# Kernel tuning notes

Hardware: AMD Instinct MI355X
Metric: run time of the kernel (lower is better)

## Reference

```python
import jax, jax.numpy as jnp
import numpy as np

N_NODES = 100000
N_EDGES = 1600000
N_FEAT = 512
HIDDEN = 128
N_CLASSES = 64
K = 10
ALPHA = 0.1


def setup_inputs() -> dict:
    key = jax.random.key(0)
    k1, k2, k3, k4 = jax.random.split(key, 4)
    x = jax.random.normal(k1, (N_NODES, N_FEAT), dtype=jnp.float32)
    edge_index = jax.random.randint(k2, (2, N_EDGES), 0, N_NODES, dtype=jnp.int64)
    W1 = jax.random.normal(k3, (N_FEAT, HIDDEN), dtype=jnp.float32) * (1.0 / np.sqrt(N_FEAT))
    b1 = jnp.zeros((HIDDEN,), dtype=jnp.float32)
    W2 = jax.random.normal(k4, (HIDDEN, N_CLASSES), dtype=jnp.float32) * (1.0 / np.sqrt(HIDDEN))
    b2 = jnp.zeros((N_CLASSES,), dtype=jnp.float32)
    return {"x": x, "edge_index": edge_index, "W1": W1, "b1": b1, "W2": W2, "b2": b2}


def reference(x, edge_index, W1, b1, W2, b2):
    N = x.shape[0]
    # MLP (dropout disabled in eval): relu(x W1 + b1) W2 + b2
    h = jax.nn.relu(x @ W1 + b1) @ W2 + b2  # [N, C]

    # GCN normalization with self-loops (APPNP default)
    loop = jnp.arange(N, dtype=edge_index.dtype)
    src = jnp.concatenate([edge_index[0], loop])  # message sources
    dst = jnp.concatenate([edge_index[1], loop])  # message targets
    deg = jax.ops.segment_sum(jnp.ones_like(src, dtype=h.dtype), dst, num_segments=N)
    dinv = jnp.where(deg > 0, jax.lax.rsqrt(deg), 0.0)
    w = (dinv[src] * dinv[dst])[:, None]  # [E+N, 1] symmetric norm

    # K-step personalized-pagerank propagation with teleport mixing
    x0 = h
    for _ in range(K):
        agg = jax.ops.segment_sum(w * h[src], dst, num_segments=N)  # \hat{A} h
        h = (1.0 - ALPHA) * agg + ALPHA * x0

    return jax.nn.log_softmax(h, axis=1)
```

## Files before the change

kernel.cpp:

```cpp
#include <hip/hip_runtime.h>
#include <hip/hip_bf16.h>

typedef __attribute__((ext_vector_type(8))) short s8v;
typedef __attribute__((ext_vector_type(4))) float f4v;

#define NNODES 100000
#define NEDGES 1600000
#define NFEAT 512
#define NHID 128
#define NCLS 64
#define NBUK 196
#define CAP 9216

static __device__ __forceinline__ short f2bf(float f) {
  __hip_bfloat16 h = __float2bfloat16(f);
  return __builtin_bit_cast(short, h);
}
static __device__ __forceinline__ float bflo(unsigned int u) {
  return __builtin_bit_cast(float, u << 16);
}
static __device__ __forceinline__ float bfhi(unsigned int u) {
  return __builtin_bit_cast(float, u & 0xFFFF0000u);
}
static __device__ __forceinline__ unsigned int pk(float lo, float hi) {
  return (unsigned int)(unsigned short)f2bf(lo) |
         ((unsigned int)(unsigned short)f2bf(hi) << 16);
}
static __device__ __forceinline__ void glds16(const void* g, void* l) {
  __builtin_amdgcn_global_load_lds(
      (const __attribute__((address_space(1))) unsigned int*)g,
      (__attribute__((address_space(3))) unsigned int*)l, 16, 0, 0);
}

static __device__ __forceinline__ bool detect32(const int* __restrict__ ei, int* sm) {
  if (threadIdx.x == 0) *sm = 0;
  __syncthreads();
  int i = threadIdx.x & 255;
  int acc = ei[2 * i + 1] | ei[2 * (i + 256) + 1] |
            ei[2 * (i + 512) + 1] | ei[2 * (i + 768) + 1];
  if (acc != 0) atomicOr(sm, 1);
  __syncthreads();
  return *sm != 0;
}

__global__ __launch_bounds__(256) void bucket_k(const int* __restrict__ ei,
                                                int* __restrict__ gcur,
                                                uint2* __restrict__ pairbuf) {
  __shared__ int sm;
  __shared__ int lcnt[NBUK], gpos[NBUK], loff[NBUK];
  bool is32 = detect32(ei, &sm);
  int t = threadIdx.x;
  int e0 = blockIdx.x * 4096;
  if (t < NBUK) lcnt[t] = 0;
  __syncthreads();
  int s_[16], d_[16];
#pragma unroll
  for (int k = 0; k < 16; ++k) {
    int e = e0 + k * 256 + t;
    int s = -1, d = -1;
    if (e < NEDGES) {
      if (is32) { s = ei[e];     d = ei[NEDGES + e]; }
      else      { s = ei[2 * e]; d = ei[2 * NEDGES + 2 * e]; }
    }
    s_[k] = s; d_[k] = d;
    if (d >= 0) atomicAdd(&lcnt[d >> 9], 1);
  }
  __syncthreads();
  if (t < NBUK) { gpos[t] = atomicAdd(&gcur[t], lcnt[t]); loff[t] = 0; }
  __syncthreads();
#pragma unroll
  for (int k = 0; k < 16; ++k) {
    int d = d_[k];
    if (d >= 0) {
      int b = d >> 9;
      int pos = gpos[b] + atomicAdd(&loff[b], 1);
      if (pos < (b + 1) * CAP) {
        uint2 p; p.x = (unsigned)s_[k]; p.y = (unsigned)d;
        pairbuf[pos] = p;
      }
    }
  }
}

__global__ __launch_bounds__(1024) void csr_k(const uint2* __restrict__ pairbuf,
                                              const int* __restrict__ gcur,
                                              int* __restrict__ rs,
                                              float* __restrict__ dinv,
                                              int* __restrict__ csrc) {
  __shared__ int lcnt[512];
  __shared__ int lscan[512];
  __shared__ int ssz[256];
  int t = threadIdx.x, b = blockIdx.x;
  int nbase = b * 512;
  if (t < 256) ssz[t] = (t < NBUK) ? (gcur[t] - t * CAP) : 0;
  if (t < 512) lcnt[t] = 0;
  __syncthreads();
  for (int off = 1; off < 256; off <<= 1) {
    int v = 0;
    if (t < 256 && t >= off) v = ssz[t - off];
    __syncthreads();
    if (t < 256) ssz[t] += v;
    __syncthreads();
  }
  int nb = gcur[b] - b * CAP;
  int gbase = (b > 0) ? ssz[b - 1] : 0;
  const uint2* mybuf = pairbuf + (size_t)b * CAP;

  for (int i = t; i < nb; i += 1024)
    atomicAdd(&lcnt[mybuf[i].y & 511], 1);
  __syncthreads();

  int c0 = (t < 512) ? lcnt[t] : 0;
  if (t < 512) lscan[t] = c0;
  __syncthreads();
  for (int off = 1; off < 512; off <<= 1) {
    int v = 0;
    if (t < 512 && t >= off) v = lscan[t - off];
    __syncthreads();
    if (t < 512) lscan[t] += v;
    __syncthreads();
  }
  int node = nbase + t;
  int r0 = 0;
  if (t < 512) {
    r0 = gbase + lscan[t] - c0;
    if (node < NNODES) { rs[node] = r0; dinv[node] = rsqrtf((float)(c0 + 1)); }
  }
  if (b == NBUK - 1 && t == 0) rs[NNODES] = NEDGES;
  __syncthreads();
  if (t < 512) lcnt[t] = r0;
  __syncthreads();

  for (int i = t; i < nb; i += 1024) {
    uint2 p = mybuf[i];
    int pos = atomicAdd(&lcnt[p.y & 511], 1);
    csrc[pos] = (int)p.x;
  }
}

__global__ __launch_bounds__(256) void wt_k(const float* __restrict__ W1, short* __restrict__ W1t,
                                            const float* __restrict__ W2, short* __restrict__ W2t,
                                            int* __restrict__ gcur) {
  if (blockIdx.x == 0 && threadIdx.x < NBUK) gcur[threadIdx.x] = threadIdx.x * CAP;
  int i = blockIdx.x * 256 + threadIdx.x;
  if (i < NFEAT * NHID) {
    int k = i >> 7, c = i & 127;
    W1t[(size_t)c * NFEAT + k] = f2bf(W1[i]);
  } else {
    int j = i - NFEAT * NHID;
    if (j < NHID * NCLS) {
      int k = j >> 6, c = j & 63;
      W2t[(size_t)c * NHID + k] = f2bf(W2[j]);
    }
  }
}

__global__ __launch_bounds__(512, 4) void mlp3_k(const float* __restrict__ x,
                                                 const short* __restrict__ W1t,
                                                 const float* __restrict__ b1,
                                                 const short* __restrict__ W2t,
                                                 const float* __restrict__ b2,
                                                 const float* __restrict__ dinv,
                                                 unsigned short* __restrict__ x0,
                                                 unsigned short* __restrict__ g0) {
  __shared__ __align__(16) short As[2][8192];
  __shared__ __align__(16) short Bs[2][8192];
  int tid = threadIdx.x, lane = tid & 63, wave = tid >> 6;
  int r = lane & 15, q = lane >> 4;
  int G = tid >> 4, li = tid & 15;
  int row0 = blockIdx.x * 128;
  int wr = (wave >> 1) * 32, wc = (wave & 1) * 64;
  char* AsB = (char*)As;
  char* BsB = (char*)Bs;

  auto loadA = [&](float4* av, int kk) {
#pragma unroll
    for (int rd = 0; rd < 4; ++rd) {
      int row = rd * 32 + G;
      int grow = row0 + row; if (grow >= NNODES) grow = NNODES - 1;
      av[rd] = *reinterpret_cast<const float4*>(x + (size_t)grow * NFEAT + kk + li * 4);
    }
  };
  auto writeA = [&](const float4* av, int buf) {
#pragma unroll
    for (int rd = 0; rd < 4; ++rd) {
      int row = rd * 32 + G;
      uint2 u;
      u.x = pk(av[rd].x, av[rd].y);
      u.y = pk(av[rd].z, av[rd].w);
      *(uint2*)(AsB + buf * 16384 + row * 128 + (((li >> 1) ^ (row & 7)) << 4) + (li & 1) * 8) = u;
    }
  };
  auto stageB = [&](int buf, int kk) {
#pragma unroll
    for (int i2 = 0; i2 < 2; ++i2) {
      int i = wave * 2 + i2;
      int col = i * 8 + (lane >> 3);
      int srcg = (lane & 7) ^ (col & 7);
      glds16(W1t + (size_t)col * NFEAT + kk + srcg * 8, BsB + buf * 16384 + i * 1024);
    }
  };

  f4v acc[2][4];
#pragma unroll
  for (int a = 0; a < 2; ++a)
#pragma unroll
    for (int b = 0; b < 4; ++b) acc[a][b] = (f4v){0.f, 0.f, 0.f, 0.f};

  {
    float4 av[4];
    loadA(av, 0);
    stageB(0, 0);
    writeA(av, 0);
  }
  __syncthreads();

  int cur = 0;
  for (int c = 0; c < 8; ++c) {
    float4 av[4];
    if (c < 7) {
      loadA(av, (c + 1) * 64);
      stageB(cur ^ 1, (c + 1) * 64);
    }
#pragma unroll
    for (int kc = 0; kc < 2; ++kc) {
      s8v af[2], bfr[4];
#pragma unroll
      for (int rt = 0; rt < 2; ++rt) {
        int arow = wr + rt * 16 + r;
        af[rt] = *(const s8v*)(AsB + cur * 16384 + arow * 128 +
                               (((kc * 4 + q) ^ (arow & 7)) << 4));
      }
#pragma unroll
      for (int ct = 0; ct < 4; ++ct) {
        int bcol = wc + ct * 16 + r;
        bfr[ct] = *(const s8v*)(BsB + cur * 16384 + bcol * 128 +
                                (((kc * 4 + q) ^ (bcol & 7)) << 4));
      }
#pragma unroll
      for (int rt = 0; rt < 2; ++rt)
#pragma unroll
        for (int ct = 0; ct < 4; ++ct)
          acc[rt][ct] = __builtin_amdgcn_mfma_f32_16x16x32_bf16(af[rt], bfr[ct], acc[rt][ct], 0, 0, 0);
    }
    if (c < 7) writeA(av, cur ^ 1);
    __syncthreads();
    cur ^= 1;
  }

  {
    float bias1[4];
#pragma unroll
    for (int ct = 0; ct < 4; ++ct) bias1[ct] = b1[wc + ct * 16 + r];
#pragma unroll
    for (int rt = 0; rt < 2; ++rt)
#pragma unroll
      for (int ct = 0; ct < 4; ++ct) {
        int col = wc + ct * 16 + r;
#pragma unroll
        for (int j = 0; j < 4; ++j) {
          int row = wr + rt * 16 + q * 4 + j;
          float v = acc[rt][ct][j] + bias1[ct];
          v = v > 0.f ? v : 0.f;
          *(short*)(AsB + row * 256 + (((col >> 3) ^ (row & 15)) << 4) + (col & 7) * 2) = f2bf(v);
        }
      }
  }
  __syncthreads();

  int wc2 = (wave & 1) * 32;
  f4v acc2[2][2];
#pragma unroll
  for (int a = 0; a < 2; ++a)
#pragma unroll
    for (int b = 0; b < 2; ++b) acc2[a][b] = (f4v){0.f, 0.f, 0.f, 0.f};
#pragma unroll
  for (int kc = 0; kc < 4; ++kc) {
    s8v a2[2], b2f[2];
#pragma unroll
    for (int rt = 0; rt < 2; ++rt) {
      int row = wr + rt * 16 + r;
      a2[rt] = *(const s8v*)(AsB + row * 256 + (((kc * 4 + q) ^ (row & 15)) << 4));
    }
#pragma unroll
    for (int ct = 0; ct < 2; ++ct) {
      int col2 = wc2 + ct * 16 + r;
      b2f[ct] = *(const s8v*)(W2t + (size_t)col2 * NHID + kc * 32 + q * 8);
    }
#pragma unroll
    for (int rt = 0; rt < 2; ++rt)
#pragma unroll
      for (int ct = 0; ct < 2; ++ct)
        acc2[rt][ct] = __builtin_amdgcn_mfma_f32_16x16x32_bf16(a2[rt], b2f[ct], acc2[rt][ct], 0, 0, 0);
  }

  {
    float bias2[2];
#pragma unroll
    for (int ct = 0; ct < 2; ++ct) bias2[ct] = b2[wc2 + ct * 16 + r];
#pragma unroll
    for (int rt = 0; rt < 2; ++rt)
#pragma unroll
      for (int j = 0; j < 4; ++j) {
        int row = wr + rt * 16 + q * 4 + j;
        int grow = row0 + row;
        float dv = dinv[grow < NNODES ? grow : NNODES - 1];
#pragma unroll
        for (int ct = 0; ct < 2; ++ct) {
          float hh = acc2[rt][ct][j] + bias2[ct];
          int col = wc2 + ct * 16 + r;
          int byte = row * 128 + (((col >> 3) ^ (row & 7)) << 4) + (col & 7) * 2;
          *(short*)(BsB + byte) = f2bf(hh);
          *(short*)(BsB + 16384 + byte) = f2bf(dv * hh);
        }
      }
  }
  __syncthreads();
#pragma unroll
  for (int rd = 0; rd < 4; ++rd) {
    int row = rd * 32 + G;
    int grow = row0 + row;
    if (grow < NNODES) {
      int byte = row * 128 + (((li >> 1) ^ (row & 7)) << 4) + (li & 1) * 8;
      uint2 vx = *(const uint2*)(BsB + byte);
      uint2 vg = *(const uint2*)(BsB + 16384 + byte);
      *(uint2*)(x0 + (size_t)grow * NCLS + li * 4) = vx;
      *(uint2*)(g0 + (size_t)grow * NCLS + li * 4) = vg;
    }
  }
}

__global__ __launch_bounds__(256) void prop_k(const unsigned short* __restrict__ gin,
                                              const unsigned short* __restrict__ x0,
                                              const float* __restrict__ dinv,
                                              const int* __restrict__ rs,
                                              const int* __restrict__ csrc,
                                              unsigned short* __restrict__ gout,
                                              float* __restrict__ out,
                                              int last) {
  int tid = threadIdx.x;
  int lane = tid & 63;
  int r = lane & 7;
  int gbase = lane & 56;
  int node = blockIdx.x * 32 + (tid >> 6) * 8 + (lane >> 3);
  int b = rs[node];
  int deg = rs[node + 1] - b;

  uint4 sv = ((const uint4*)(gin + (size_t)node * NCLS))[r];
  uint4 xv = ((const uint4*)(x0 + (size_t)node * NCLS))[r];
  float dvn = dinv[node];

  float a0 = bflo(sv.x), a1 = bfhi(sv.x), a2 = bflo(sv.y), a3 = bfhi(sv.y);
  float a4 = bflo(sv.z), a5 = bfhi(sv.z), a6 = bflo(sv.w), a7 = bfhi(sv.w);

  int m = deg;
  m = max(m, __shfl_xor(m, 8));
  m = max(m, __shfl_xor(m, 16));
  m = max(m, __shfl_xor(m, 32));

  int idx = NNODES;
  if (r < deg) idx = csrc[b + r];
  for (int basek = 0; basek < m; basek += 8) {
    int nidx = NNODES;
    if (basek + 8 + r < deg) nidx = csrc[b + basek + 8 + r];
#pragma unroll
    for (int j = 0; j < 8; ++j) {
      int sj = __shfl(idx, gbase + j);
      uint4 v = ((const uint4*)(gin + (size_t)sj * NCLS))[r];
      a0 += bflo(v.x); a1 += bfhi(v.x); a2 += bflo(v.y); a3 += bfhi(v.y);
      a4 += bflo(v.z); a5 += bfhi(v.z); a6 += bflo(v.w); a7 += bfhi(v.w);
    }
    idx = nidx;
  }

  float h0 = 0.9f * (dvn * a0) + 0.1f * bflo(xv.x);
  float h1 = 0.9f * (dvn * a1) + 0.1f * bfhi(xv.x);
  float h2 = 0.9f * (dvn * a2) + 0.1f * bflo(xv.y);
  float h3 = 0.9f * (dvn * a3) + 0.1f * bfhi(xv.y);
  float h4 = 0.9f * (dvn * a4) + 0.1f * bflo(xv.z);
  float h5 = 0.9f * (dvn * a5) + 0.1f * bfhi(xv.z);
  float h6 = 0.9f * (dvn * a6) + 0.1f * bflo(xv.w);
  float h7 = 0.9f * (dvn * a7) + 0.1f * bfhi(xv.w);

  if (!last) {
    uint4 o;
    o.x = pk(dvn * h0, dvn * h1);
    o.y = pk(dvn * h2, dvn * h3);
    o.z = pk(dvn * h4, dvn * h5);
    o.w = pk(dvn * h6, dvn * h7);
    ((uint4*)(gout + (size_t)node * NCLS))[r] = o;
  } else {
    float mx = fmaxf(fmaxf(fmaxf(h0, h1), fmaxf(h2, h3)),
                     fmaxf(fmaxf(h4, h5), fmaxf(h6, h7)));
#pragma unroll
    for (int off = 1; off < 8; off <<= 1) mx = fmaxf(mx, __shfl_xor(mx, off));
    float s = __expf(h0 - mx) + __expf(h1 - mx) + __expf(h2 - mx) + __expf(h3 - mx) +
              __expf(h4 - mx) + __expf(h5 - mx) + __expf(h6 - mx) + __expf(h7 - mx);
#pragma unroll
    for (int off = 1; off < 8; off <<= 1) s += __shfl_xor(s, off);
    float ls = __logf(s);
    float* op = out + (size_t)node * NCLS + r * 8;
    float4 o0 = {h0 - mx - ls, h1 - mx - ls, h2 - mx - ls, h3 - mx - ls};
    float4 o1 = {h4 - mx - ls, h5 - mx - ls, h6 - mx - ls, h7 - mx - ls};
    *(float4*)(op) = o0;
    *(float4*)(op + 4) = o1;
  }
}

extern "C" void kernel_launch(void* const* d_in, const int* in_sizes, int n_in,
                              void* d_out, int out_size, void* d_ws, size_t ws_size,
                              hipStream_t stream) {
  const float* x  = (const float*)d_in[0];
  const int*   ei = (const int*)d_in[1];
  const float* W1 = (const float*)d_in[2];
  const float* b1 = (const float*)d_in[3];
  const float* W2 = (const float*)d_in[4];
  const float* b2 = (const float*)d_in[5];

  char* ws = (char*)d_ws;
  unsigned short* x0bf   = (unsigned short*)(ws);
  uint2*          pairbuf= (uint2*)(ws);
  unsigned short* gA     = (unsigned short*)(ws + 12800000);
  unsigned short* gB     = (unsigned short*)(ws + 25600256);
  int*            csrc   = (int*)(ws + 38400384);
  int*            rs     = (int*)(ws + 45200384);
  float*          dinv   = (float*)(ws + 46000512);
  short*          W1t    = (short*)(ws + 46800512);
  short*          W2t    = (short*)(ws + 46931584);
  int*            gcur   = (int*)(ws + 46950144);

  hipMemsetAsync((char*)gA + (size_t)NNODES * NCLS * 2, 0, 128, stream);
  hipMemsetAsync((char*)gB + (size_t)NNODES * NCLS * 2, 0, 128, stream);

  wt_k<<<(NFEAT * NHID + NHID * NCLS + 255) / 256, 256, 0, stream>>>(W1, W1t, W2, W2t, gcur);
  bucket_k<<<(NEDGES + 4095) / 4096, 256, 0, stream>>>(ei, gcur, pairbuf);
  csr_k<<<NBUK, 1024, 0, stream>>>(pairbuf, gcur, rs, dinv, csrc);

  mlp3_k<<<(NNODES + 127) / 128, 512, 0, stream>>>(x, W1t, b1, W2t, b2, dinv, x0bf, gB);

  for (int t = 1; t <= 10; ++t) {
    const unsigned short* gin = (t & 1) ? gB : gA;
    unsigned short* gout      = (t & 1) ? gA : gB;
    prop_k<<<NNODES / 32, 256, 0, stream>>>(gin, x0bf, dinv, rs, csrc, gout,
                                            (float*)d_out, t == 10);
  }
}
```

Before: 404.5 us.

## Split propagation features into 16-column blocks for cache-resident gathers

Reorganizes the bf16 propagation buffers into four column blocks of 16 features per node, and assigns each prop block one column block so that the gathered working set (about 3.2 MB per block) fits better in L2/MALL. Each node is now handled by two lanes with 16-byte loads, and the edge index reads are split across those two lanes. The log-softmax is moved into a separate kernel that reads the final bf16 state, and the padding memsets are folded into the weight transpose kernel. In exchange, each edge's index is now read four times (once per column block), and there is an extra launch plus a bf16 rounding of the final state before the softmax.

```diff
diff --git a/kernel.cpp b/kernel.cpp
--- a/kernel.cpp
+++ b/kernel.cpp
@@ -11,6 +11,7 @@
 #define NCLS 64
 #define NBUK 196
 #define CAP 9216
+#define CBS ((NNODES + 1) * 16)
 
 static __device__ __forceinline__ short f2bf(float f) {
   __hip_bfloat16 h = __float2bfloat16(f);
@@ -140,8 +141,16 @@
 
 __global__ __launch_bounds__(256) void wt_k(const float* __restrict__ W1, short* __restrict__ W1t,
                                             const float* __restrict__ W2, short* __restrict__ W2t,
-                                            int* __restrict__ gcur) {
+                                            int* __restrict__ gcur,
+                                            unsigned short* __restrict__ gA,
+                                            unsigned short* __restrict__ gB) {
   if (blockIdx.x == 0 && threadIdx.x < NBUK) gcur[threadIdx.x] = threadIdx.x * CAP;
+  if (blockIdx.x == 1 && threadIdx.x < 128) {
+    int t = threadIdx.x;
+    unsigned short* p = (t >> 6) ? gB : gA;
+    int c = (t >> 4) & 3, sh = t & 15;
+    p[(size_t)c * CBS + (size_t)NNODES * 16 + sh] = 0;
+  }
   int i = blockIdx.x * 256 + threadIdx.x;
   if (i < NFEAT * NHID) {
     int k = i >> 7, c = i & 127;
@@ -324,8 +333,9 @@
       int byte = row * 128 + (((li >> 1) ^ (row & 7)) << 4) + (li & 1) * 8;
       uint2 vx = *(const uint2*)(BsB + byte);
       uint2 vg = *(const uint2*)(BsB + 16384 + byte);
-      *(uint2*)(x0 + (size_t)grow * NCLS + li * 4) = vx;
-      *(uint2*)(g0 + (size_t)grow * NCLS + li * 4) = vg;
+      size_t dst = (size_t)(li >> 2) * CBS + (size_t)grow * 16 + (li & 3) * 4;
+      *(uint2*)(x0 + dst) = vx;
+      *(uint2*)(g0 + dst) = vg;
     }
   }
 }
@@ -336,41 +346,50 @@
                                               const int* __restrict__ rs,
                                               const int* __restrict__ csrc,
                                               unsigned short* __restrict__ gout,
-                                              float* __restrict__ out,
                                               int last) {
+  int bid = blockIdx.x;
+  int cb = (bid & 7) >> 1;
+  int nodeblk = (bid >> 3) * 2 + (bid & 1);
   int tid = threadIdx.x;
-  int lane = tid & 63;
-  int r = lane & 7;
-  int gbase = lane & 56;
-  int node = blockIdx.x * 32 + (tid >> 6) * 8 + (lane >> 3);
+  int lane = tid & 63, wave = tid >> 6;
+  int half = lane & 1;
+  int node = nodeblk * 128 + wave * 32 + (lane >> 1);
+  if (node >= NNODES) node = NNODES - 1;
   int b = rs[node];
   int deg = rs[node + 1] - b;
 
-  uint4 sv = ((const uint4*)(gin + (size_t)node * NCLS))[r];
-  uint4 xv = ((const uint4*)(x0 + (size_t)node * NCLS))[r];
+  const unsigned short* gcb = gin + (size_t)cb * CBS;
+  uint4 sv = *(const uint4*)(gcb + (size_t)node * 16 + half * 8);
+  uint4 xv = *(const uint4*)(x0 + (size_t)cb * CBS + (size_t)node * 16 + half * 8);
   float dvn = dinv[node];
 
   float a0 = bflo(sv.x), a1 = bfhi(sv.x), a2 = bflo(sv.y), a3 = bfhi(sv.y);
   float a4 = bflo(sv.z), a5 = bfhi(sv.z), a6 = bflo(sv.w), a7 = bfhi(sv.w);
 
   int m = deg;
+  m = max(m, __shfl_xor(m, 2));
+  m = max(m, __shfl_xor(m, 4));
   m = max(m, __shfl_xor(m, 8));
   m = max(m, __shfl_xor(m, 16));
   m = max(m, __shfl_xor(m, 32));
 
-  int idx = NNODES;
-  if (r < deg) idx = csrc[b + r];
   for (int basek = 0; basek < m; basek += 8) {
-    int nidx = NNODES;
-    if (basek + 8 + r < deg) nidx = csrc[b + basek + 8 + r];
-#pragma unroll
-    for (int j = 0; j < 8; ++j) {
-      int sj = __shfl(idx, gbase + j);
-      uint4 v = ((const uint4*)(gin + (size_t)sj * NCLS))[r];
-      a0 += bflo(v.x); a1 += bfhi(v.x); a2 += bflo(v.y); a3 += bfhi(v.y);
-      a4 += bflo(v.z); a5 += bfhi(v.z); a6 += bflo(v.w); a7 += bfhi(v.w);
-    }
-    idx = nidx;
+    if (basek < deg) {
+      int i0 = b + basek + half * 4;
+      int idx[4];
+#pragma unroll
+      for (int u = 0; u < 4; ++u) {
+        int e = basek + half * 4 + u;
+        idx[u] = (e < deg) ? csrc[i0 + u] : NNODES;
+      }
+#pragma unroll
+      for (int j = 0; j < 8; ++j) {
+        int sj = __shfl(idx[j & 3], (lane & 62) + (j >> 2));
+        uint4 v = *(const uint4*)(gcb + (size_t)sj * 16 + half * 8);
+        a0 += bflo(v.x); a1 += bfhi(v.x); a2 += bflo(v.y); a3 += bfhi(v.y);
+        a4 += bflo(v.z); a5 += bfhi(v.z); a6 += bflo(v.w); a7 += bfhi(v.w);
+      }
+    }
   }
 
   float h0 = 0.9f * (dvn * a0) + 0.1f * bflo(xv.x);
@@ -382,29 +401,38 @@
   float h6 = 0.9f * (dvn * a6) + 0.1f * bflo(xv.w);
   float h7 = 0.9f * (dvn * a7) + 0.1f * bfhi(xv.w);
 
-  if (!last) {
-    uint4 o;
-    o.x = pk(dvn * h0, dvn * h1);
-    o.y = pk(dvn * h2, dvn * h3);
-    o.z = pk(dvn * h4, dvn * h5);
-    o.w = pk(dvn * h6, dvn * h7);
-    ((uint4*)(gout + (size_t)node * NCLS))[r] = o;
-  } else {
-    float mx = fmaxf(fmaxf(fmaxf(h0, h1), fmaxf(h2, h3)),
-                     fmaxf(fmaxf(h4, h5), fmaxf(h6, h7)));
-#pragma unroll
-    for (int off = 1; off < 8; off <<= 1) mx = fmaxf(mx, __shfl_xor(mx, off));
-    float s = __expf(h0 - mx) + __expf(h1 - mx) + __expf(h2 - mx) + __expf(h3 - mx) +
-              __expf(h4 - mx) + __expf(h5 - mx) + __expf(h6 - mx) + __expf(h7 - mx);
-#pragma unroll
-    for (int off = 1; off < 8; off <<= 1) s += __shfl_xor(s, off);
-    float ls = __logf(s);
-    float* op = out + (size_t)node * NCLS + r * 8;
-    float4 o0 = {h0 - mx - ls, h1 - mx - ls, h2 - mx - ls, h3 - mx - ls};
-    float4 o1 = {h4 - mx - ls, h5 - mx - ls, h6 - mx - ls, h7 - mx - ls};
-    *(float4*)(op) = o0;
-    *(float4*)(op + 4) = o1;
-  }
+  float s0 = last ? h0 : dvn * h0, s1 = last ? h1 : dvn * h1;
+  float s2 = last ? h2 : dvn * h2, s3 = last ? h3 : dvn * h3;
+  float s4 = last ? h4 : dvn * h4, s5 = last ? h5 : dvn * h5;
+  float s6 = last ? h6 : dvn * h6, s7 = last ? h7 : dvn * h7;
+  uint4 o;
+  o.x = pk(s0, s1); o.y = pk(s2, s3); o.z = pk(s4, s5); o.w = pk(s6, s7);
+  *(uint4*)(gout + (size_t)cb * CBS + (size_t)node * 16 + half * 8) = o;
+}
+
+__global__ __launch_bounds__(256) void softmax_k(const unsigned short* __restrict__ hbm,
+                                                 float* __restrict__ out) {
+  int tid = threadIdx.x;
+  int lane = tid & 63;
+  int r = lane & 7;
+  int node = blockIdx.x * 32 + (tid >> 6) * 8 + (lane >> 3);
+  uint4 v = *(const uint4*)(hbm + (size_t)(r >> 1) * CBS + (size_t)node * 16 + (r & 1) * 8);
+  float h0 = bflo(v.x), h1 = bfhi(v.x), h2 = bflo(v.y), h3 = bfhi(v.y);
+  float h4 = bflo(v.z), h5 = bfhi(v.z), h6 = bflo(v.w), h7 = bfhi(v.w);
+  float mx = fmaxf(fmaxf(fmaxf(h0, h1), fmaxf(h2, h3)),
+                   fmaxf(fmaxf(h4, h5), fmaxf(h6, h7)));
+#pragma unroll
+  for (int off = 1; off < 8; off <<= 1) mx = fmaxf(mx, __shfl_xor(mx, off));
+  float s = __expf(h0 - mx) + __expf(h1 - mx) + __expf(h2 - mx) + __expf(h3 - mx) +
+            __expf(h4 - mx) + __expf(h5 - mx) + __expf(h6 - mx) + __expf(h7 - mx);
+#pragma unroll
+  for (int off = 1; off < 8; off <<= 1) s += __shfl_xor(s, off);
+  float ls = __logf(s);
+  float* op = out + (size_t)node * NCLS + r * 8;
+  float4 o0 = {h0 - mx - ls, h1 - mx - ls, h2 - mx - ls, h3 - mx - ls};
+  float4 o1 = {h4 - mx - ls, h5 - mx - ls, h6 - mx - ls, h7 - mx - ls};
+  *(float4*)(op) = o0;
+  *(float4*)(op + 4) = o1;
 }
 
 extern "C" void kernel_launch(void* const* d_in, const int* in_sizes, int n_in,
@@ -420,19 +448,17 @@
   char* ws = (char*)d_ws;
   unsigned short* x0bf   = (unsigned short*)(ws);
   uint2*          pairbuf= (uint2*)(ws);
-  unsigned short* gA     = (unsigned short*)(ws + 12800000);
+  unsigned short* gA     = (unsigned short*)(ws + 12800128);
   unsigned short* gB     = (unsigned short*)(ws + 25600256);
   int*            csrc   = (int*)(ws + 38400384);
-  int*            rs     = (int*)(ws + 45200384);
-  float*          dinv   = (float*)(ws + 46000512);
-  short*          W1t    = (short*)(ws + 46800512);
-  short*          W2t    = (short*)(ws + 46931584);
-  int*            gcur   = (int*)(ws + 46950144);
-
-  hipMemsetAsync((char*)gA + (size_t)NNODES * NCLS * 2, 0, 128, stream);
-  hipMemsetAsync((char*)gB + (size_t)NNODES * NCLS * 2, 0, 128, stream);
-
-  wt_k<<<(NFEAT * NHID + NHID * NCLS + 255) / 256, 256, 0, stream>>>(W1, W1t, W2, W2t, gcur);
+  int*            rs     = (int*)(ws + 44800384);
+  float*          dinv   = (float*)(ws + 45200512);
+  short*          W1t    = (short*)(ws + 45600512);
+  short*          W2t    = (short*)(ws + 45731584);
+  int*            gcur   = (int*)(ws + 45747968);
+
+  wt_k<<<(NFEAT * NHID + NHID * NCLS + 255) / 256, 256, 0, stream>>>(W1, W1t, W2, W2t,
+                                                                     gcur, gA, gB);
   bucket_k<<<(NEDGES + 4095) / 4096, 256, 0, stream>>>(ei, gcur, pairbuf);
   csr_k<<<NBUK, 1024, 0, stream>>>(pairbuf, gcur, rs, dinv, csrc);
 
@@ -441,7 +467,7 @@
   for (int t = 1; t <= 10; ++t) {
     const unsigned short* gin = (t & 1) ? gB : gA;
     unsigned short* gout      = (t & 1) ? gA : gB;
-    prop_k<<<NNODES / 32, 256, 0, stream>>>(gin, x0bf, dinv, rs, csrc, gout,
-                                            (float*)d_out, t == 10);
-  }
-}
+    prop_k<<<3128, 256, 0, stream>>>(gin, x0bf, dinv, rs, csrc, gout, t == 10);
+  }
+  softmax_k<<<NNODES / 32, 256, 0, stream>>>(gB, (float*)d_out);
+}
```

Measured after the change: 560.6 us. 1.39x slower.
